# Optimization experiments

Hardware: AMD Instinct MI355X
Metric: run time of the kernel (lower is better)

## Reference

```python
import jax, jax.numpy as jnp
from jax import lax
import numpy as np

SR = 48000
NUM_BANDS = 12
IR_LEN = 32768          # reverb impulse-response length in samples
NUM_TAPS = 511          # bandpass FIR length for the noise filterbank
BS, CHS, T = 32, 2, 131072
EPS = 1e-8


def make_filterbank():
    """12-band windowed-sinc bandpass filterbank spanning 0..Nyquist."""
    n = np.arange(NUM_TAPS) - (NUM_TAPS - 1) / 2.0
    win = np.hamming(NUM_TAPS)
    filts = []
    for b in range(NUM_BANDS):
        lo = 0.5 * b / NUM_BANDS
        hi = 0.5 * (b + 1) / NUM_BANDS
        h = 2.0 * hi * np.sinc(2.0 * hi * n) - 2.0 * lo * np.sinc(2.0 * lo * n)
        filts.append(h * win)
    return np.stack(filts).astype(np.float32)  # (12, NUM_TAPS)


def _distortion(x, drive_db):
    # tanh waveshaper with dB drive gain
    return jnp.tanh(x * 10.0 ** (drive_db / 20.0))


def _compressor(x, thr, ratio, atk_ms, rel_ms, knee, makeup):
    # soft-knee gain computer in dB domain
    x_db = 20.0 * jnp.log10(jnp.abs(x) + EPS)          # (bs, chs, T)
    knee = jnp.maximum(knee, 1e-3)
    over = x_db - thr
    g_knee = x_db + (1.0 / ratio - 1.0) * (over + knee / 2.0) ** 2 / (2.0 * knee)
    g = jnp.where(2.0 * over < -knee, x_db,
                  jnp.where(2.0 * over > knee, thr + over / ratio, g_knee))
    gain_db = g - x_db                                  # desired gain reduction (<= 0)
    # per-sample attack/release one-pole envelope follower (sequential scan)
    alpha_a = jnp.exp(-1.0 / (SR * atk_ms / 1000.0))
    alpha_r = jnp.exp(-1.0 / (SR * rel_ms / 1000.0))
    g_t = jnp.moveaxis(gain_db, -1, 0)                  # (T, bs, chs)

    def step(prev, cur):
        alpha = jnp.where(cur < prev, alpha_a, alpha_r)  # attack when reduction grows
        new = alpha * prev + (1.0 - alpha) * cur
        return new, new

    _, smooth = lax.scan(step, jnp.zeros(g_t.shape[1:], x.dtype), g_t)
    smooth = jnp.moveaxis(smooth, 0, -1)                # (bs, chs, T)
    return x * 10.0 ** ((smooth + makeup) / 20.0)


def _reverb(x, band_gains, band_decays, mix, noise, fir_bank):
    bs, chs, seq = x.shape
    n = noise.reshape(bs * chs, NUM_BANDS, -1)          # (N, 12, IR_LEN+TAPS-1)
    # grouped conv: each band of noise filtered by its bandpass FIR
    filt = lax.conv_general_dilated(
        n, fir_bank[:, None, :], (1,), 'VALID',
        dimension_numbers=('NCH', 'OIH', 'NCH'),
        feature_group_count=NUM_BANDS)                  # (N, 12, IR_LEN)
    t = jnp.linspace(0.0, 1.0, IR_LEN, dtype=x.dtype)
    d = band_decays * 10.0 + 1.0
    env = jnp.exp(-d[:, None] * t[None, :])             # (12, IR_LEN) decay envelopes
    ir = jnp.mean(filt * (env * band_gains[:, None]), axis=1)  # (N, IR_LEN)
    ir = ir.reshape(bs, chs, IR_LEN)
    # FFT convolution of input with the synthesized IR
    nfft = seq + IR_LEN - 1
    wet = jnp.fft.irfft(jnp.fft.rfft(x, nfft) * jnp.fft.rfft(ir, nfft), nfft)[..., :seq]
    return (1.0 - mix) * x + mix * wet


def _forward(x, drive, thr, ratio, atk, rel, knee, makeup, mix,
             band_gains, band_decays, noise, fir_bank):
    x = _distortion(x, drive)
    x = _compressor(x, thr, ratio, atk, rel, knee, makeup)
    return _reverb(x, band_gains, band_decays, mix, noise, fir_bank)


def setup_inputs() -> dict:
    key = jax.random.key(0)
    k1, k2 = jax.random.split(key)
    return {
        "x": 0.5 * jax.random.normal(k1, (BS, CHS, T), jnp.float32),
        "drive": jnp.float32(5.0),
        "threshold_db": jnp.float32(-20.0),
        "ratio": jnp.float32(4.0),
        "attack_ms": jnp.float32(10.0),
        "release_ms": jnp.float32(50.0),
        "knee_db": jnp.float32(6.0),
        "makeup_gain_db": jnp.float32(0.0),
        "mix": jnp.float32(0.3),
        "band_gains": jnp.zeros((NUM_BANDS,), jnp.float32),
        "band_decays": 0.5 * jnp.ones((NUM_BANDS,), jnp.float32),
        "noise": jax.random.normal(k2, (BS, CHS, NUM_BANDS, IR_LEN + NUM_TAPS - 1), jnp.float32),
        "fir_bank": jnp.asarray(make_filterbank()),
    }


def reference(x, drive, threshold_db, ratio, attack_ms, release_ms, knee_db,
              makeup_gain_db, mix, band_gains, band_decays, noise, fir_bank):
    return _forward(x, drive, threshold_db, ratio, attack_ms, release_ms,
                    knee_db, makeup_gain_db, mix, band_gains, band_decays,
                    noise, fir_bank)
```

## Files before the change

kernel.cpp:

```cpp
#include <hip/hip_runtime.h>
#include <math.h>
#include <stdint.h>

#define NCHW    64
#define TLEN    131072
#define IRLEN   32768
#define NTAPS   511
#define NBANDS  12
#define NOISELEN (IRLEN + NTAPS - 1)

#define WUP     4096
#define CHK     256
#define NCHUNK  (TLEN / CHK)

#define K10     0.16609640474436813f
#define DB2     6.0205999132796239f

__device__ __forceinline__ float fast_tanh(float z) {
    float az = fabsf(z);
    float e  = exp2f(az * 2.8853900817779268f);
    float r  = 1.0f - 2.0f / (e + 1.0f);
    return copysignf(r, z);
}

__device__ __forceinline__ float gain_db_one(float xs, float g, float thr,
                                             float q, float knee, float inv2k) {
    float y    = fast_tanh(xs * g);
    float a    = fabsf(y) + 1e-8f;
    float xdb  = __log2f(a) * DB2;
    float over = xdb - thr;
    float h    = over + 0.5f * knee;
    float gk   = q * h * h * inv2k;
    float t2   = 2.0f * over;
    return (t2 < -knee) ? 0.0f : ((t2 > knee) ? q * over : gk);
}

__global__ __launch_bounds__(256) void k1_gain(
    const float* __restrict__ x,
    const float* __restrict__ p_drive, const float* __restrict__ p_thr,
    const float* __restrict__ p_ratio, const float* __restrict__ p_knee,
    const float* __restrict__ p_atk,   const float* __restrict__ band_gains,
    float* __restrict__ acur2, int* __restrict__ flag)
{
    if (blockIdx.x == 0 && threadIdx.x == 0) {
        int f = 0;
        #pragma unroll
        for (int b = 0; b < NBANDS; ++b) f |= (band_gains[b] != 0.0f) ? 1 : 0;
        *flag = f;
    }
    __shared__ float S[64 * 65];
    int t0 = blockIdx.x * 64;
    int l  = threadIdx.x & 63;
    int w  = threadIdx.x >> 6;

    float g     = exp2f(p_drive[0] * K10);
    float thr   = p_thr[0];
    float knee  = fmaxf(p_knee[0], 1e-3f);
    float q     = 1.0f / p_ratio[0] - 1.0f;
    float inv2k = 1.0f / (2.0f * knee);
    float aa    = expf(-1.0f / (48.0f * p_atk[0]));
    float omaa  = 1.0f - aa;

    #pragma unroll
    for (int i = 0; i < 16; ++i) {
        int ch = w * 16 + i;
        float xv = x[(size_t)ch * TLEN + t0 + l];
        S[l * 65 + ch] = omaa * gain_db_one(xv, g, thr, q, knee, inv2k);
    }
    __syncthreads();

    float4* dst = (float4*)(acur2 + (size_t)t0 * 64);
    #pragma unroll
    for (int i = 0; i < 4; ++i) {
        int gq = threadIdx.x + 256 * i;
        int s2 = gq >> 5;
        int cp = (gq & 31) * 2;
        float4 v;
        v.x = S[(2 * s2)     * 65 + cp];
        v.y = S[(2 * s2 + 1) * 65 + cp];
        v.z = S[(2 * s2)     * 65 + cp + 1];
        v.w = S[(2 * s2 + 1) * 65 + cp + 1];
        dst[gq] = v;
    }
}

#define ROWS   64
#define TILEF  (ROWS * 128)

__device__ __forceinline__ void stage_tile(const float* __restrict__ gsrc,
                                           float* lds_dst, int lane) {
    #pragma unroll
    for (int c = 0; c < 32; ++c) {
        __builtin_amdgcn_global_load_lds(
            (const __attribute__((address_space(1))) void*)(gsrc + c * 256 + lane * 4),
            (__attribute__((address_space(3))) void*)(lds_dst + c * 256),
            16, 0, 0);
    }
}

__global__ __launch_bounds__(128) void k2_env(
    const float* __restrict__ acur2,
    const float* __restrict__ p_atk, const float* __restrict__ p_rel,
    float* __restrict__ smooth2)
{
    __shared__ float lds[2 * TILEF];
    int b    = blockIdx.x;
    int j    = ((b & 7) << 6) | (b >> 3);
    int lane = threadIdx.x & 63;
    int wv   = threadIdx.x >> 6;

    float aa  = expf(-1.0f / (48.0f * p_atk[0]));
    float ar  = expf(-1.0f / (48.0f * p_rel[0]));
    float rho = (1.0f - ar) / (1.0f - aa);

    int t0   = (j >= WUP / CHK) ? (j * CHK - WUP) : 0;
    int te   = j * CHK;
    int th0  = t0 >> 1, the = te >> 1, thend = (te + CHK) >> 1;
    int nt   = (thend - th0) / ROWS;
    int ot   = (the - th0) / ROWS;

    const float* gbase = acur2 + (size_t)th0 * 128;
    float2* d2 = (float2*)smooth2 + lane;

    if (wv == 1) stage_tile(gbase, lds, lane);

    float p = 0.0f;
    for (int tl = 0; tl < nt; ++tl) {
        __syncthreads();
        int buf = (tl & 1) ? TILEF : 0;
        if (wv == 1) {
            if (tl + 1 < nt)
                stage_tile(gbase + (size_t)(tl + 1) * TILEF,
                           lds + (TILEF - buf), lane);
        } else {
            const float* L = lds + buf + lane * 2;
            int thb = th0 + tl * ROWS;
            if (tl >= ot) {
                #pragma unroll
                for (int u = 0; u < ROWS; ++u) {
                    float2 a = *(const float2*)(L + u * 128);
                    float fa = fmaf(aa, p, a.x);
                    float fr = fmaf(ar, p, rho * a.x);
                    p = fminf(fa, fr);
                    float2 o; o.x = p;
                    fa = fmaf(aa, p, a.y);
                    fr = fmaf(ar, p, rho * a.y);
                    p = fminf(fa, fr);
                    o.y = p;
                    d2[(size_t)(thb + u) * 64] = o;
                }
            } else {
                #pragma unroll
                for (int u = 0; u < ROWS; ++u) {
                    float2 a = *(const float2*)(L + u * 128);
                    float fa = fmaf(aa, p, a.x);
                    float fr = fmaf(ar, p, rho * a.x);
                    p = fminf(fa, fr);
                    fa = fmaf(aa, p, a.y);
                    fr = fmaf(ar, p, rho * a.y);
                    p = fminf(fa, fr);
                }
            }
        }
    }
}

__global__ __launch_bounds__(256) void k3_out(
    const float* __restrict__ x, const float* __restrict__ smooth2,
    const float* __restrict__ p_drive, const float* __restrict__ p_makeup,
    const float* __restrict__ p_mix, const int* __restrict__ flag,
    float* __restrict__ out, float* __restrict__ comp)
{
    __shared__ float S[32 * 130];
    __shared__ int sflag;
    if (threadIdx.x == 0) sflag = *flag;
    int t0 = blockIdx.x * 64;

    const float4* src = (const float4*)(smooth2 + (size_t)t0 * 64);
    #pragma unroll
    for (int i = 0; i < 4; ++i) {
        int f4 = threadIdx.x + 256 * i;
        float4 v = src[f4];
        int f   = f4 * 4;
        float* d = S + (f >> 7) * 130 + (f & 127);
        d[0] = v.x; d[1] = v.y; d[2] = v.z; d[3] = v.w;
    }
    __syncthreads();

    int l = threadIdx.x & 63, w = threadIdx.x >> 6;
    float g   = exp2f(p_drive[0] * K10);
    float mk  = p_makeup[0];
    float mix = p_mix[0];
    float dry = 1.0f - mix;
    int f = sflag;

    #pragma unroll
    for (int i = 0; i < 16; ++i) {
        int ch = w * 16 + i;
        float sm = S[(l >> 1) * 130 + ch * 2 + (l & 1)];
        size_t idx = (size_t)ch * TLEN + t0 + l;
        float cv = fast_tanh(x[idx] * g) * exp2f((sm + mk) * K10);
        out[idx] = dry * cv;
        if (f) comp[idx] = cv;
    }
}

__global__ __launch_bounds__(256) void k4_ir(
    const float* __restrict__ noise, const float* __restrict__ fir,
    const float* __restrict__ gains, const float* __restrict__ decays,
    const int* __restrict__ flag, float* __restrict__ ir)
{
    __shared__ int sflag;
    if (threadIdx.x == 0) sflag = *flag;
    __syncthreads();
    if (!sflag) return;
    __shared__ float sf[NBANDS * NTAPS];
    for (int i = threadIdx.x; i < NBANDS * NTAPS; i += 256) sf[i] = fir[i];
    __syncthreads();
    size_t total  = (size_t)NCHW * IRLEN;
    size_t stride = (size_t)gridDim.x * 256;
    for (size_t idx = blockIdx.x * 256 + threadIdx.x; idx < total; idx += stride) {
        int nch = (int)(idx >> 15);
        int n   = (int)(idx & (IRLEN - 1));
        float tl  = n * (1.0f / (IRLEN - 1));
        float acc = 0.0f;
        for (int bb = 0; bb < NBANDS; ++bb) {
            float gb = gains[bb];
            if (gb == 0.0f) continue;
            float env = expf(-(decays[bb] * 10.0f + 1.0f) * tl) * gb;
            const float* np_ = noise + ((size_t)nch * NBANDS + bb) * NOISELEN + n;
            const float* fb  = sf + bb * NTAPS;
            float s = 0.0f;
            for (int k = 0; k < NTAPS; ++k) s = fmaf(np_[k], fb[k], s);
            acc = fmaf(env, s, acc);
        }
        ir[idx] = acc * (1.0f / NBANDS);
    }
}

__global__ __launch_bounds__(256) void k5_wet(
    const float* __restrict__ comp, const float* __restrict__ ir,
    const float* __restrict__ p_mix, const int* __restrict__ flag,
    float* __restrict__ out)
{
    __shared__ int sflag;
    if (threadIdx.x == 0) sflag = *flag;
    __syncthreads();
    if (!sflag) return;
    float mix = p_mix[0];
    size_t total  = (size_t)NCHW * TLEN;
    size_t stride = (size_t)gridDim.x * 256;
    for (size_t idx = blockIdx.x * 256 + threadIdx.x; idx < total; idx += stride) {
        int nch = (int)(idx >> 17);
        int t   = (int)(idx & (TLEN - 1));
        const float* c   = comp + (size_t)nch * TLEN;
        const float* irp = ir + (size_t)nch * IRLEN;
        int kmax = (t < IRLEN - 1) ? t : (IRLEN - 1);
        float s = 0.0f;
        for (int k = 0; k <= kmax; ++k) s = fmaf(irp[k], c[t - k], s);
        out[idx] += mix * s;
    }
}

extern "C" void kernel_launch(void* const* d_in, const int* in_sizes, int n_in,
                              void* d_out, int out_size, void* d_ws, size_t ws_size,
                              hipStream_t stream)
{
    const float* x      = (const float*)d_in[0];
    const float* drive  = (const float*)d_in[1];
    const float* thr    = (const float*)d_in[2];
    const float* ratio  = (const float*)d_in[3];
    const float* atk    = (const float*)d_in[4];
    const float* rel    = (const float*)d_in[5];
    const float* knee   = (const float*)d_in[6];
    const float* makeup = (const float*)d_in[7];
    const float* mix    = (const float*)d_in[8];
    const float* bg     = (const float*)d_in[9];
    const float* bd     = (const float*)d_in[10];
    const float* noise  = (const float*)d_in[11];
    const float* fir    = (const float*)d_in[12];
    float* out = (float*)d_out;

    char*  w       = (char*)d_ws;
    int*   flag    = (int*)w;
    float* acur2   = (float*)(w + 16);
    float* smooth2 = acur2 + (size_t)NCHW * TLEN;
    float* ir      = smooth2 + (size_t)NCHW * TLEN;
    float* comp    = acur2;

    k1_gain<<<TLEN / 64, 256, 0, stream>>>(x, drive, thr, ratio, knee, atk, bg, acur2, flag);
    k2_env<<<NCHUNK, 128, 0, stream>>>(acur2, atk, rel, smooth2);
    k3_out<<<TLEN / 64, 256, 0, stream>>>(x, smooth2, drive, makeup, mix, flag, out, comp);
    k4_ir<<<1024, 256, 0, stream>>>(noise, fir, bg, bd, flag, ir);
    k5_wet<<<1024, 256, 0, stream>>>(comp, ir, mix, flag, out);
}
```

Baseline: 256.4 us.

## Precompose 4-step envelope maps in gain kernel and fuse output stage into scan

The gain kernel now composes the min-of-two-affine envelope step over each group of 4 samples into a 5-term min-of-affine map. The warmup scan therefore advances 4 samples per iteration using precomputed coefficients. The output stage (tanh, gain apply, dry mix, comp write) is fused into the envelope kernel through an LDS buffer, which removes the smooth-array round trip and one kernel launch. In exchange, workspace traffic grows (q4/q1/pq arrays), chunk size doubles, and the IR/wet grids shrink.

New measurement: 253.3 us. Within noise of the previous version (-1.2%).

```diff
diff --git a/kernel.cpp b/kernel.cpp
--- a/kernel.cpp
+++ b/kernel.cpp
@@ -10,8 +10,10 @@
 #define NOISELEN (IRLEN + NTAPS - 1)
 
 #define WUP     4096
-#define CHK     256
-#define NCHUNK  (TLEN / CHK)
+#define CHK     512
+#define NBLK2   (TLEN / CHK)
+#define NQ      (TLEN / 4)
+#define GRP     16
 
 #define K10     0.16609640474436813f
 #define DB2     6.0205999132796239f
@@ -35,12 +37,18 @@
     return (t2 < -knee) ? 0.0f : ((t2 > knee) ? q * over : gk);
 }
 
+__device__ __forceinline__ float f4c(const float4& v, int s) {
+    return s == 0 ? v.x : (s == 1 ? v.y : (s == 2 ? v.z : v.w));
+}
+
 __global__ __launch_bounds__(256) void k1_gain(
     const float* __restrict__ x,
     const float* __restrict__ p_drive, const float* __restrict__ p_thr,
     const float* __restrict__ p_ratio, const float* __restrict__ p_knee,
-    const float* __restrict__ p_atk,   const float* __restrict__ band_gains,
-    float* __restrict__ acur2, int* __restrict__ flag)
+    const float* __restrict__ p_atk,   const float* __restrict__ p_rel,
+    const float* __restrict__ band_gains,
+    float4* __restrict__ q4, float* __restrict__ q1, float4* __restrict__ pq,
+    int* __restrict__ flag)
 {
     if (blockIdx.x == 0 && threadIdx.x == 0) {
         int f = 0;
@@ -56,152 +64,180 @@
     float g     = exp2f(p_drive[0] * K10);
     float thr   = p_thr[0];
     float knee  = fmaxf(p_knee[0], 1e-3f);
-    float q     = 1.0f / p_ratio[0] - 1.0f;
+    float qr    = 1.0f / p_ratio[0] - 1.0f;
     float inv2k = 1.0f / (2.0f * knee);
     float aa    = expf(-1.0f / (48.0f * p_atk[0]));
+    float ar    = expf(-1.0f / (48.0f * p_rel[0]));
     float omaa  = 1.0f - aa;
+    float rho   = (1.0f - ar) / omaa;
 
     #pragma unroll
     for (int i = 0; i < 16; ++i) {
         int ch = w * 16 + i;
         float xv = x[(size_t)ch * TLEN + t0 + l];
-        S[l * 65 + ch] = omaa * gain_db_one(xv, g, thr, q, knee, inv2k);
+        S[l * 65 + ch] = omaa * gain_db_one(xv, g, thr, qr, knee, inv2k);
     }
     __syncthreads();
 
-    float4* dst = (float4*)(acur2 + (size_t)t0 * 64);
+    int ch = threadIdx.x & 63;
+    int ql = threadIdx.x >> 6;
     #pragma unroll
-    for (int i = 0; i < 4; ++i) {
-        int gq = threadIdx.x + 256 * i;
-        int s2 = gq >> 5;
-        int cp = (gq & 31) * 2;
-        float4 v;
-        v.x = S[(2 * s2)     * 65 + cp];
-        v.y = S[(2 * s2 + 1) * 65 + cp];
-        v.z = S[(2 * s2)     * 65 + cp + 1];
-        v.w = S[(2 * s2 + 1) * 65 + cp + 1];
-        dst[gq] = v;
-    }
-}
-
-#define ROWS   64
-#define TILEF  (ROWS * 128)
-
-__device__ __forceinline__ void stage_tile(const float* __restrict__ gsrc,
-                                           float* lds_dst, int lane) {
-    #pragma unroll
-    for (int c = 0; c < 32; ++c) {
-        __builtin_amdgcn_global_load_lds(
-            (const __attribute__((address_space(1))) void*)(gsrc + c * 256 + lane * 4),
-            (__attribute__((address_space(3))) void*)(lds_dst + c * 256),
-            16, 0, 0);
-    }
-}
-
-__global__ __launch_bounds__(128) void k2_env(
-    const float* __restrict__ acur2,
+    for (int k = 0; k < 4; ++k) {
+        int qq = ql * 4 + k;
+        int sb = qq * 4;
+        float A0 = S[(sb + 0) * 65 + ch];
+        float A1 = S[(sb + 1) * 65 + ch];
+        float A2 = S[(sb + 2) * 65 + ch];
+        float A3 = S[(sb + 3) * 65 + ch];
+        float R0 = rho * A0, R1 = rho * A1, R2 = rho * A2, R3 = rho * A3;
+        float i0 = A0, i1 = R0;
+        float n0 = fmaf(aa, i0, A1);
+        float n1 = fminf(fmaf(aa, i1, A1), fmaf(ar, i0, R1));
+        float n2 = fmaf(ar, i1, R1);
+        float m0 = fmaf(aa, n0, A2);
+        float m1 = fminf(fmaf(aa, n1, A2), fmaf(ar, n0, R2));
+        float m2 = fminf(fmaf(aa, n2, A2), fmaf(ar, n1, R2));
+        float m3 = fmaf(ar, n2, R2);
+        float o0 = fmaf(aa, m0, A3);
+        float o1 = fminf(fmaf(aa, m1, A3), fmaf(ar, m0, R3));
+        float o2 = fminf(fmaf(aa, m2, A3), fmaf(ar, m1, R3));
+        float o3 = fminf(fmaf(aa, m3, A3), fmaf(ar, m2, R3));
+        float o4 = fmaf(ar, m3, R3);
+        size_t gi = (size_t)(blockIdx.x * 16 + qq) * 64 + ch;
+        q4[gi] = make_float4(o0, o1, o2, o3);
+        q1[gi] = o4;
+        pq[gi] = make_float4(A0, A1, A2, A3);
+    }
+}
+
+#define WSTEP(c4, c1s) { \
+    float f0 = fmaf(s0, p, (c4).x); \
+    float f1 = fmaf(s1, p, (c4).y); \
+    float f2 = fmaf(s2, p, (c4).z); \
+    float f3 = fmaf(s3, p, (c4).w); \
+    float f4 = fmaf(s4, p, (c1s)); \
+    p = fminf(fminf(fminf(f0, f1), f2), fminf(f3, f4)); \
+}
+
+#define ESTEP(Av, tl) { \
+    float fa = fmaf(aa, p, (Av)); \
+    float fr = fmaf(ar, p, rho * (Av)); \
+    p = fminf(fa, fr); \
+    Ssm[(tl) * 68 + lane] = p; \
+}
+
+#define APPLY(xv, tq, cq) { \
+    float4 sm0 = *(const float4*)&Ssm[(4 * (tq) + 0) * 68 + (cq) * 4]; \
+    float4 sm1 = *(const float4*)&Ssm[(4 * (tq) + 1) * 68 + (cq) * 4]; \
+    float4 sm2 = *(const float4*)&Ssm[(4 * (tq) + 2) * 68 + (cq) * 4]; \
+    float4 sm3 = *(const float4*)&Ssm[(4 * (tq) + 3) * 68 + (cq) * 4]; \
+    _Pragma("unroll") \
+    for (int cc = 0; cc < 4; ++cc) { \
+        float c0 = fast_tanh(f4c(xv[cc], 0) * g) * exp2f((f4c(sm0, cc) + mk) * K10); \
+        float c1 = fast_tanh(f4c(xv[cc], 1) * g) * exp2f((f4c(sm1, cc) + mk) * K10); \
+        float c2 = fast_tanh(f4c(xv[cc], 2) * g) * exp2f((f4c(sm2, cc) + mk) * K10); \
+        float c3 = fast_tanh(f4c(xv[cc], 3) * g) * exp2f((f4c(sm3, cc) + mk) * K10); \
+        size_t oidx = (size_t)((cq) * 4 + cc) * TLEN + tb + 4 * (tq); \
+        *(float4*)&out[oidx] = make_float4(dry * c0, dry * c1, dry * c2, dry * c3); \
+        if (sflag) *(float4*)&comp[oidx] = make_float4(c0, c1, c2, c3); \
+    } \
+}
+
+__global__ __launch_bounds__(256, 1) void k2_env(
+    const float* __restrict__ x,
+    const float4* __restrict__ q4, const float* __restrict__ q1,
+    const float4* __restrict__ pq,
     const float* __restrict__ p_atk, const float* __restrict__ p_rel,
-    float* __restrict__ smooth2)
-{
-    __shared__ float lds[2 * TILEF];
-    int b    = blockIdx.x;
-    int j    = ((b & 7) << 6) | (b >> 3);
-    int lane = threadIdx.x & 63;
-    int wv   = threadIdx.x >> 6;
+    const float* __restrict__ p_drive, const float* __restrict__ p_makeup,
+    const float* __restrict__ p_mix, const int* __restrict__ flag,
+    float* __restrict__ out, float* __restrict__ comp)
+{
+    __shared__ __attribute__((aligned(16))) float Ssm[128 * 68];
+    __shared__ int sflag;
+    int tid = threadIdx.x;
+    if (tid == 0) sflag = *flag;
+
+    int b  = blockIdx.x;
+    int j  = ((b & 7) << 5) | (b >> 3);
+    int te = j * CHK;
+    int t0 = (j >= WUP / CHK) ? te - WUP : 0;
+    int q0 = t0 >> 2, qe = te >> 2;
+    int lane = tid & 63;
 
     float aa  = expf(-1.0f / (48.0f * p_atk[0]));
     float ar  = expf(-1.0f / (48.0f * p_rel[0]));
     float rho = (1.0f - ar) / (1.0f - aa);
-
-    int t0   = (j >= WUP / CHK) ? (j * CHK - WUP) : 0;
-    int te   = j * CHK;
-    int th0  = t0 >> 1, the = te >> 1, thend = (te + CHK) >> 1;
-    int nt   = (thend - th0) / ROWS;
-    int ot   = (the - th0) / ROWS;
-
-    const float* gbase = acur2 + (size_t)th0 * 128;
-    float2* d2 = (float2*)smooth2 + lane;
-
-    if (wv == 1) stage_tile(gbase, lds, lane);
-
-    float p = 0.0f;
-    for (int tl = 0; tl < nt; ++tl) {
-        __syncthreads();
-        int buf = (tl & 1) ? TILEF : 0;
-        if (wv == 1) {
-            if (tl + 1 < nt)
-                stage_tile(gbase + (size_t)(tl + 1) * TILEF,
-                           lds + (TILEF - buf), lane);
-        } else {
-            const float* L = lds + buf + lane * 2;
-            int thb = th0 + tl * ROWS;
-            if (tl >= ot) {
-                #pragma unroll
-                for (int u = 0; u < ROWS; ++u) {
-                    float2 a = *(const float2*)(L + u * 128);
-                    float fa = fmaf(aa, p, a.x);
-                    float fr = fmaf(ar, p, rho * a.x);
-                    p = fminf(fa, fr);
-                    float2 o; o.x = p;
-                    fa = fmaf(aa, p, a.y);
-                    fr = fmaf(ar, p, rho * a.y);
-                    p = fminf(fa, fr);
-                    o.y = p;
-                    d2[(size_t)(thb + u) * 64] = o;
-                }
-            } else {
-                #pragma unroll
-                for (int u = 0; u < ROWS; ++u) {
-                    float2 a = *(const float2*)(L + u * 128);
-                    float fa = fmaf(aa, p, a.x);
-                    float fr = fmaf(ar, p, rho * a.x);
-                    p = fminf(fa, fr);
-                    fa = fmaf(aa, p, a.y);
-                    fr = fmaf(ar, p, rho * a.y);
-                    p = fminf(fa, fr);
-                }
-            }
-        }
-    }
-}
-
-__global__ __launch_bounds__(256) void k3_out(
-    const float* __restrict__ x, const float* __restrict__ smooth2,
-    const float* __restrict__ p_drive, const float* __restrict__ p_makeup,
-    const float* __restrict__ p_mix, const int* __restrict__ flag,
-    float* __restrict__ out, float* __restrict__ comp)
-{
-    __shared__ float S[32 * 130];
-    __shared__ int sflag;
-    if (threadIdx.x == 0) sflag = *flag;
-    int t0 = blockIdx.x * 64;
-
-    const float4* src = (const float4*)(smooth2 + (size_t)t0 * 64);
-    #pragma unroll
-    for (int i = 0; i < 4; ++i) {
-        int f4 = threadIdx.x + 256 * i;
-        float4 v = src[f4];
-        int f   = f4 * 4;
-        float* d = S + (f >> 7) * 130 + (f & 127);
-        d[0] = v.x; d[1] = v.y; d[2] = v.z; d[3] = v.w;
-    }
-    __syncthreads();
-
-    int l = threadIdx.x & 63, w = threadIdx.x >> 6;
+    float s0 = aa * aa * aa * aa, s1 = aa * aa * aa * ar, s2 = aa * aa * ar * ar,
+          s3 = aa * ar * ar * ar, s4 = ar * ar * ar * ar;
     float g   = exp2f(p_drive[0] * K10);
     float mk  = p_makeup[0];
     float mix = p_mix[0];
     float dry = 1.0f - mix;
-    int f = sflag;
-
-    #pragma unroll
-    for (int i = 0; i < 16; ++i) {
-        int ch = w * 16 + i;
-        float sm = S[(l >> 1) * 130 + ch * 2 + (l & 1)];
-        size_t idx = (size_t)ch * TLEN + t0 + l;
-        float cv = fast_tanh(x[idx] * g) * exp2f((sm + mk) * K10);
-        out[idx] = dry * cv;
-        if (f) comp[idx] = cv;
+
+    float p = 0.0f;
+
+    if (tid < 64 && qe > q0) {
+        float4 A4[GRP]; float A1v[GRP]; float4 B4[GRP]; float B1v[GRP];
+        size_t base = (size_t)q0 * 64 + lane;
+        #pragma unroll
+        for (int u = 0; u < GRP; ++u) {
+            A4[u]  = q4[base + (size_t)u * 64];
+            A1v[u] = q1[base + (size_t)u * 64];
+        }
+        for (int gq = q0; gq < qe; gq += 2 * GRP) {
+            size_t bb = (size_t)(gq + GRP) * 64 + lane;
+            #pragma unroll
+            for (int u = 0; u < GRP; ++u) {
+                B4[u]  = q4[bb + (size_t)u * 64];
+                B1v[u] = q1[bb + (size_t)u * 64];
+            }
+            #pragma unroll
+            for (int u = 0; u < GRP; ++u) WSTEP(A4[u], A1v[u]);
+            size_t ab = (size_t)(gq + 2 * GRP) * 64 + lane;
+            #pragma unroll
+            for (int u = 0; u < GRP; ++u) {
+                A4[u]  = q4[ab + (size_t)u * 64];
+                A1v[u] = q1[ab + (size_t)u * 64];
+            }
+            #pragma unroll
+            for (int u = 0; u < GRP; ++u) WSTEP(B4[u], B1v[u]);
+        }
+    }
+
+    int tqa = tid & 31,         cqa = tid >> 5;
+    int tqb = (tid + 256) & 31, cqb = (tid + 256) >> 5;
+
+    for (int r = 0; r < 4; ++r) {
+        int tb = te + r * 128;
+        float4 xva[4], xvb[4];
+        #pragma unroll
+        for (int cc = 0; cc < 4; ++cc) {
+            xva[cc] = *(const float4*)&x[(size_t)(cqa * 4 + cc) * TLEN + tb + 4 * tqa];
+            xvb[cc] = *(const float4*)&x[(size_t)(cqb * 4 + cc) * TLEN + tb + 4 * tqb];
+        }
+        if (tid < 64) {
+            float4 C4[GRP], D4[GRP];
+            size_t eb = (size_t)(qe + r * 32) * 64 + lane;
+            #pragma unroll
+            for (int u = 0; u < GRP; ++u) C4[u] = pq[eb + (size_t)u * 64];
+            #pragma unroll
+            for (int u = 0; u < GRP; ++u) D4[u] = pq[eb + (size_t)(u + GRP) * 64];
+            #pragma unroll
+            for (int u = 0; u < GRP; ++u) {
+                ESTEP(C4[u].x, u * 4 + 0); ESTEP(C4[u].y, u * 4 + 1);
+                ESTEP(C4[u].z, u * 4 + 2); ESTEP(C4[u].w, u * 4 + 3);
+            }
+            #pragma unroll
+            for (int u = 0; u < GRP; ++u) {
+                int t4 = (u + GRP) * 4;
+                ESTEP(D4[u].x, t4 + 0); ESTEP(D4[u].y, t4 + 1);
+                ESTEP(D4[u].z, t4 + 2); ESTEP(D4[u].w, t4 + 3);
+            }
+        }
+        __syncthreads();
+        APPLY(xva, tqa, cqa);
+        APPLY(xvb, tqb, cqb);
+        __syncthreads();
     }
 }
 
@@ -281,16 +317,18 @@
     const float* fir    = (const float*)d_in[12];
     float* out = (float*)d_out;
 
-    char*  w       = (char*)d_ws;
-    int*   flag    = (int*)w;
-    float* acur2   = (float*)(w + 16);
-    float* smooth2 = acur2 + (size_t)NCHW * TLEN;
-    float* ir      = smooth2 + (size_t)NCHW * TLEN;
-    float* comp    = acur2;
-
-    k1_gain<<<TLEN / 64, 256, 0, stream>>>(x, drive, thr, ratio, knee, atk, bg, acur2, flag);
-    k2_env<<<NCHUNK, 128, 0, stream>>>(acur2, atk, rel, smooth2);
-    k3_out<<<TLEN / 64, 256, 0, stream>>>(x, smooth2, drive, makeup, mix, flag, out, comp);
-    k4_ir<<<1024, 256, 0, stream>>>(noise, fir, bg, bd, flag, ir);
-    k5_wet<<<1024, 256, 0, stream>>>(comp, ir, mix, flag, out);
-}
+    char*  w    = (char*)d_ws;
+    int*   flag = (int*)w;
+    float* q4f  = (float*)(w + 16);
+    float* q1f  = q4f + (size_t)NQ * 256;
+    float* pqf  = q1f + (size_t)NQ * 64;
+    float* cmp  = pqf + (size_t)NQ * 256;
+    float* ir   = cmp + (size_t)NCHW * TLEN;
+
+    k1_gain<<<TLEN / 64, 256, 0, stream>>>(x, drive, thr, ratio, knee, atk, rel,
+                                           bg, (float4*)q4f, q1f, (float4*)pqf, flag);
+    k2_env<<<NBLK2, 256, 0, stream>>>(x, (const float4*)q4f, q1f, (const float4*)pqf,
+                                      atk, rel, drive, makeup, mix, flag, out, cmp);
+    k4_ir<<<256, 256, 0, stream>>>(noise, fir, bg, bd, flag, ir);
+    k5_wet<<<256, 256, 0, stream>>>(cmp, ir, mix, flag, out);
+}
```
